# Optimization experiments

Hardware: AMD Instinct MI355X
Metric: run time of the kernel (lower is better)

The kernel has to match this reference:

```python
import jax, jax.numpy as jnp
import numpy as np

D_MODEL = 1024
H = 16
D_K = D_MODEL // H
SEQ = 4096
SIM_WEIGHT = 1.0


def setup_inputs() -> dict:
    key = jax.random.key(0)
    ks = jax.random.split(key, 10)
    s = 1.0 / np.sqrt(D_MODEL)
    return {
        "x": jax.random.normal(ks[0], (SEQ, D_MODEL), dtype=jnp.float32),
        "similarity_matrix": jax.random.normal(ks[1], (SEQ, SEQ), dtype=jnp.float32),
        "w_q": jax.random.normal(ks[2], (D_MODEL, D_MODEL), dtype=jnp.float32) * s,
        "b_q": jnp.zeros((D_MODEL,), dtype=jnp.float32),
        "w_k": jax.random.normal(ks[3], (D_MODEL, D_MODEL), dtype=jnp.float32) * s,
        "b_k": jnp.zeros((D_MODEL,), dtype=jnp.float32),
        "w_v": jax.random.normal(ks[4], (D_MODEL, D_MODEL), dtype=jnp.float32) * s,
        "b_v": jnp.zeros((D_MODEL,), dtype=jnp.float32),
        "w_o": jax.random.normal(ks[5], (D_MODEL, D_MODEL), dtype=jnp.float32) * s,
        "b_o": jnp.zeros((D_MODEL,), dtype=jnp.float32),
    }


def reference(x, similarity_matrix, w_q, b_q, w_k, b_k, w_v, b_v, w_o, b_o):
    # x: [S, D]; project and split heads -> [H, S, d_k]
    q = (x @ w_q.T + b_q).reshape(SEQ, H, D_K).transpose(1, 0, 2)
    k = (x @ w_k.T + b_k).reshape(SEQ, H, D_K).transpose(1, 0, 2)
    v = (x @ w_v.T + b_v).reshape(SEQ, H, D_K).transpose(1, 0, 2)
    # scores: [H, S, S]; additive similarity bias broadcast over heads
    scores = jnp.einsum("hsd,htd->hst", q, k) / jnp.sqrt(jnp.float32(D_K))
    scores = scores + similarity_matrix[None, :, :] * SIM_WEIGHT
    attn = jax.nn.softmax(scores, axis=-1)
    out = jnp.einsum("hst,htd->hsd", attn, v)  # [H, S, d_k]
    out = out.transpose(1, 0, 2).reshape(SEQ, D_MODEL)
    return out @ w_o.T + b_o
```

## Files before the change

kernel.cpp:

```cpp
#include <hip/hip_runtime.h>
#include <hip/hip_bf16.h>

typedef __hip_bfloat16 bf16;
typedef __attribute__((ext_vector_type(8))) short short8;
typedef __attribute__((ext_vector_type(4))) float f32x4;

#define SEQ    4096
#define DMODEL 1024
#define NHEAD  16
#define DKH    64

#define LSTRIDE 72
#define PSTRIDE 72

__device__ __forceinline__ float ldf(const float* p, size_t i) { return p[i]; }
__device__ __forceinline__ float ldf(const bf16*  p, size_t i) { return __bfloat162float(p[i]); }
__device__ __forceinline__ void stf(float* p, size_t i, float v) { p[i] = v; }
__device__ __forceinline__ void stf(bf16*  p, size_t i, float v) { p[i] = __float2bfloat16(v); }

__device__ __forceinline__ short f2bs(float v) {
    bf16 b = __float2bfloat16(v);
    return *(short*)&b;
}

__device__ __forceinline__ short8 lda8(const bf16* p, size_t i) {
    return *(const short8*)(p + i);
}
__device__ __forceinline__ short8 lda8(const float* p, size_t i) {
    float4 a = *(const float4*)(p + i);
    float4 b = *(const float4*)(p + i + 4);
    short8 r;
    r[0] = f2bs(a.x); r[1] = f2bs(a.y); r[2] = f2bs(a.z); r[3] = f2bs(a.w);
    r[4] = f2bs(b.x); r[5] = f2bs(b.y); r[6] = f2bs(b.z); r[7] = f2bs(b.w);
    return r;
}

__device__ __forceinline__ void g2l16(const void* g, void* l) {
    __builtin_amdgcn_global_load_lds(
        (const __attribute__((address_space(1))) unsigned int*)g,
        (__attribute__((address_space(3))) unsigned int*)l, 16, 0, 0);
}

__global__ void detect_dtype(const unsigned short* __restrict__ x, int* __restrict__ flag) {
    int lane = threadIdx.x;
    int cnt = 0;
    for (int i = lane; i < 512; i += 64) {
        int e = (x[i] >> 7) & 0xFF;
        cnt += (e >= 100 && e <= 140) ? 1 : 0;
    }
    #pragma unroll
    for (int off = 32; off; off >>= 1) cnt += __shfl_xor(cnt, off, 64);
    if (lane == 0) *flag = (cnt >= 400) ? 1 : 0;
}

template <bool TRANSC, typename TC>
__device__ void gemm_dma_body(const bf16* __restrict__ A, const bf16* __restrict__ B,
                              const bf16* __restrict__ bias, TC* __restrict__ C,
                              int M, int N, int K, short* As, short* Bs) {
    const int tid = threadIdx.x;
    const int w = tid >> 6, lane = tid & 63, q = lane >> 4, c = lane & 15;
    const int m0 = blockIdx.x * 128, n0 = blockIdx.y * 128;
    const int mb = 64 * (w & 1), nb = 64 * (w >> 1);

    f32x4 acc[4][4] = {};

    for (int k0 = 0; k0 < K; k0 += 64) {
        __syncthreads();
        #pragma unroll
        for (int i = 0; i < 4; ++i) {
            int p = i * 256 + tid;
            int row = p >> 3, pc = p & 7, gc = pc ^ (row & 7);
            g2l16(A + (size_t)(m0 + row) * K + k0 + gc * 8, As + (size_t)p * 8);
            g2l16(B + (size_t)(n0 + row) * K + k0 + gc * 8, Bs + (size_t)p * 8);
        }
        __syncthreads();
        #pragma unroll
        for (int kh = 0; kh < 2; ++kh) {
            short8 af[4], bfr[4];
            #pragma unroll
            for (int i = 0; i < 4; ++i) {
                int row = mb + i * 16 + c;
                af[i] = *(const short8*)&As[row * 64 + (((kh * 4 + q) ^ (row & 7)) << 3)];
            }
            #pragma unroll
            for (int j = 0; j < 4; ++j) {
                int row = nb + j * 16 + c;
                bfr[j] = *(const short8*)&Bs[row * 64 + (((kh * 4 + q) ^ (row & 7)) << 3)];
            }
            #pragma unroll
            for (int i = 0; i < 4; ++i)
                #pragma unroll
                for (int j = 0; j < 4; ++j)
                    acc[i][j] = __builtin_amdgcn_mfma_f32_16x16x32_bf16(af[i], bfr[j], acc[i][j], 0, 0, 0);
        }
    }

    #pragma unroll
    for (int j = 0; j < 4; ++j) {
        int n = n0 + nb + j * 16 + c;
        float bj = __bfloat162float(bias[n]);
        #pragma unroll
        for (int i = 0; i < 4; ++i) {
            if (TRANSC) {
                short4 pk;
                pk.x = f2bs(acc[i][j][0] + bj);
                pk.y = f2bs(acc[i][j][1] + bj);
                pk.z = f2bs(acc[i][j][2] + bj);
                pk.w = f2bs(acc[i][j][3] + bj);
                int m = m0 + mb + i * 16 + q * 4;
                *(short4*)&((bf16*)C)[(size_t)n * M + m] = pk;
            } else {
                #pragma unroll
                for (int t = 0; t < 4; ++t) {
                    int m = m0 + mb + i * 16 + q * 4 + t;
                    stf(C, (size_t)m * N + n, acc[i][j][t] + bj);
                }
            }
        }
    }
}

template <typename TA, typename TB, typename TC, bool TRANSC>
__device__ void gemm_legacy_body(const TA* __restrict__ A, const TB* __restrict__ B,
                                 const TB* __restrict__ bias, TC* __restrict__ C,
                                 int M, int N, int K, short* As, short* Bs) {
    const int tid = threadIdx.x;
    const int w = tid >> 6, lane = tid & 63, q = lane >> 4, c = lane & 15;
    const int m0 = blockIdx.x * 128, n0 = blockIdx.y * 128;
    const int mb = 64 * (w & 1), nb = 64 * (w >> 1);

    f32x4 acc[4][4] = {};

    for (int k0 = 0; k0 < K; k0 += 64) {
        __syncthreads();
        #pragma unroll
        for (int i = 0; i < 4; ++i) {
            int ch = tid + 256 * i;
            int r = ch >> 3, c8 = (ch & 7) * 8;
            *(short8*)&As[r * LSTRIDE + c8] = lda8(A, (size_t)(m0 + r) * K + k0 + c8);
            *(short8*)&Bs[r * LSTRIDE + c8] = lda8(B, (size_t)(n0 + r) * K + k0 + c8);
        }
        __syncthreads();
        #pragma unroll
        for (int kh = 0; kh < 2; ++kh) {
            const int kk = kh * 32 + q * 8;
            short8 af[4], bfr[4];
            #pragma unroll
            for (int i = 0; i < 4; ++i)
                af[i] = *(const short8*)&As[(mb + i * 16 + c) * LSTRIDE + kk];
            #pragma unroll
            for (int j = 0; j < 4; ++j)
                bfr[j] = *(const short8*)&Bs[(nb + j * 16 + c) * LSTRIDE + kk];
            #pragma unroll
            for (int i = 0; i < 4; ++i)
                #pragma unroll
                for (int j = 0; j < 4; ++j)
                    acc[i][j] = __builtin_amdgcn_mfma_f32_16x16x32_bf16(af[i], bfr[j], acc[i][j], 0, 0, 0);
        }
    }

    #pragma unroll
    for (int j = 0; j < 4; ++j) {
        int n = n0 + nb + j * 16 + c;
        float bj = ldf(bias, (size_t)n);
        #pragma unroll
        for (int i = 0; i < 4; ++i) {
            if (TRANSC) {
                short4 pk;
                pk.x = f2bs(acc[i][j][0] + bj);
                pk.y = f2bs(acc[i][j][1] + bj);
                pk.z = f2bs(acc[i][j][2] + bj);
                pk.w = f2bs(acc[i][j][3] + bj);
                int m = m0 + mb + i * 16 + q * 4;
                *(short4*)&((bf16*)C)[(size_t)n * M + m] = pk;
            } else {
                #pragma unroll
                for (int t = 0; t < 4; ++t) {
                    int m = m0 + mb + i * 16 + q * 4 + t;
                    stf(C, (size_t)m * N + n, acc[i][j][t] + bj);
                }
            }
        }
    }
}

__global__ __launch_bounds__(256)
void gemm_proj(const void* __restrict__ A, const void* __restrict__ B,
               const void* __restrict__ bias, bf16* __restrict__ C,
               const int* __restrict__ flag, int M, int N, int K) {
    __shared__ __align__(16) short As[128 * LSTRIDE];
    __shared__ __align__(16) short Bs[128 * LSTRIDE];
    if (*flag)
        gemm_dma_body<false, bf16>((const bf16*)A, (const bf16*)B, (const bf16*)bias, C, M, N, K, As, Bs);
    else
        gemm_legacy_body<float, float, bf16, false>((const float*)A, (const float*)B, (const float*)bias, C, M, N, K, As, Bs);
}

__global__ __launch_bounds__(256)
void gemm_projT(const void* __restrict__ A, const void* __restrict__ B,
                const void* __restrict__ bias, bf16* __restrict__ C,
                const int* __restrict__ flag, int M, int N, int K) {
    __shared__ __align__(16) short As[128 * LSTRIDE];
    __shared__ __align__(16) short Bs[128 * LSTRIDE];
    if (*flag)
        gemm_dma_body<true, bf16>((const bf16*)A, (const bf16*)B, (const bf16*)bias, C, M, N, K, As, Bs);
    else
        gemm_legacy_body<float, float, bf16, true>((const float*)A, (const float*)B, (const float*)bias, C, M, N, K, As, Bs);
}

__global__ __launch_bounds__(256)
void gemm_out(const bf16* __restrict__ A, const void* __restrict__ B,
              const void* __restrict__ bias, void* __restrict__ C,
              const int* __restrict__ flag, int M, int N, int K) {
    __shared__ __align__(16) short As[128 * LSTRIDE];
    __shared__ __align__(16) short Bs[128 * LSTRIDE];
    if (*flag)
        gemm_dma_body<false, bf16>(A, (const bf16*)B, (const bf16*)bias, (bf16*)C, M, N, K, As, Bs);
    else
        gemm_legacy_body<bf16, float, float, false>(A, (const float*)B, (const float*)bias, (float*)C, M, N, K, As, Bs);
}

template <typename TS>
__device__ void flash_body(const bf16* __restrict__ Q, const bf16* __restrict__ Kg,
                           const bf16* __restrict__ VtG, const TS* __restrict__ sim,
                           bf16* __restrict__ O, short* Ps) {
    const int tid = threadIdx.x;
    const int w = tid >> 6, lane = tid & 63, q = lane >> 4, c = lane & 15;
    const int q0 = blockIdx.x * 128, hd = blockIdx.y * DKH;
    const int r0 = q0 + w * 32;

    short8 aq[2][2];
    #pragma unroll
    for (int m = 0; m < 2; ++m)
        #pragma unroll
        for (int kc = 0; kc < 2; ++kc)
            aq[m][kc] = *(const short8*)&Q[(size_t)(r0 + m * 16 + c) * DMODEL + hd + kc * 32 + q * 8];

    const TS* simp[2][4];
    #pragma unroll
    for (int m = 0; m < 2; ++m)
        #pragma unroll
        for (int i = 0; i < 4; ++i)
            simp[m][i] = sim + (size_t)(r0 + m * 16 + q * 4 + i) * SEQ + c;

    f32x4 accO[2][4] = {};
    float Lp[2][4] = {};

    for (int t = 0; t < SEQ / 64; ++t) {
        const int k0 = t * 64;

        short8 bk[4][2];
        #pragma unroll
        for (int f = 0; f < 4; ++f)
            #pragma unroll
            for (int kc = 0; kc < 2; ++kc)
                bk[f][kc] = *(const short8*)&Kg[(size_t)(k0 + f * 16 + c) * DMODEL + hd + kc * 32 + q * 8];

        f32x4 sfr[2][4];
        #pragma unroll
        for (int m = 0; m < 2; ++m)
            #pragma unroll
            for (int f = 0; f < 4; ++f) {
                f32x4 a = {};
                a = __builtin_amdgcn_mfma_f32_16x16x32_bf16(aq[m][0], bk[f][0], a, 0, 0, 0);
                a = __builtin_amdgcn_mfma_f32_16x16x32_bf16(aq[m][1], bk[f][1], a, 0, 0, 0);
                sfr[m][f] = a;
            }

        #pragma unroll
        for (int m = 0; m < 2; ++m)
            #pragma unroll
            for (int f = 0; f < 4; ++f)
                #pragma unroll
                for (int i = 0; i < 4; ++i) {
                    float s = sfr[m][f][i] * 0.125f + ldf(simp[m][i], (size_t)k0 + f * 16);
                    float p = __expf(s);
                    Lp[m][i] += p;
                    Ps[(w * 32 + m * 16 + q * 4 + i) * PSTRIDE + f * 16 + c] = f2bs(p);
                }

        short8 bv[4][2];
        #pragma unroll
        for (int f = 0; f < 4; ++f)
            #pragma unroll
            for (int kc = 0; kc < 2; ++kc)
                bv[f][kc] = *(const short8*)&VtG[(size_t)(hd + f * 16 + c) * SEQ + k0 + kc * 32 + q * 8];

        short8 ap[2][2];
        #pragma unroll
        for (int m = 0; m < 2; ++m)
            #pragma unroll
            for (int kc = 0; kc < 2; ++kc)
                ap[m][kc] = *(const short8*)&Ps[(w * 32 + m * 16 + c) * PSTRIDE + kc * 32 + q * 8];

        #pragma unroll
        for (int m = 0; m < 2; ++m)
            #pragma unroll
            for (int f = 0; f < 4; ++f) {
                accO[m][f] = __builtin_amdgcn_mfma_f32_16x16x32_bf16(ap[m][0], bv[f][0], accO[m][f], 0, 0, 0);
                accO[m][f] = __builtin_amdgcn_mfma_f32_16x16x32_bf16(ap[m][1], bv[f][1], accO[m][f], 0, 0, 0);
            }
    }

    #pragma unroll
    for (int off = 1; off < 16; off <<= 1)
        #pragma unroll
        for (int m = 0; m < 2; ++m)
            #pragma unroll
            for (int i = 0; i < 4; ++i)
                Lp[m][i] += __shfl_xor(Lp[m][i], off, 64);

    #pragma unroll
    for (int m = 0; m < 2; ++m)
        #pragma unroll
        for (int i = 0; i < 4; ++i) {
            float inv = 1.f / Lp[m][i];
            int gr = r0 + m * 16 + q * 4 + i;
            #pragma unroll
            for (int f = 0; f < 4; ++f)
                O[(size_t)gr * DMODEL + hd + f * 16 + c] = __float2bfloat16(accO[m][f][i] * inv);
        }
}

__global__ __launch_bounds__(256)
void flash_mfma(const bf16* __restrict__ Q, const bf16* __restrict__ K,
                const bf16* __restrict__ Vt, const void* __restrict__ sim,
                bf16* __restrict__ O, const int* __restrict__ flag) {
    __shared__ __align__(16) short Ps[128 * PSTRIDE];
    if (*flag)
        flash_body<bf16>(Q, K, Vt, (const bf16*)sim, O, Ps);
    else
        flash_body<float>(Q, K, Vt, (const float*)sim, O, Ps);
}

extern "C" void kernel_launch(void* const* d_in, const int* in_sizes, int n_in,
                              void* d_out, int out_size, void* d_ws, size_t ws_size,
                              hipStream_t stream) {
    int* flagw = (int*)d_ws;
    const int* flag = (const int*)d_ws;
    bf16* Q  = (bf16*)((char*)d_ws + 256);
    bf16* K  = Q + (size_t)SEQ * DMODEL;
    bf16* Vt = K + (size_t)SEQ * DMODEL;
    bf16* O  = Vt + (size_t)SEQ * DMODEL;

    detect_dtype<<<1, 64, 0, stream>>>((const unsigned short*)d_in[0], flagw);

    dim3 gg(SEQ / 128, DMODEL / 128);
    dim3 blk(256);
    gemm_proj <<<gg, blk, 0, stream>>>(d_in[0], d_in[2], d_in[3], Q,  flag, SEQ, DMODEL, DMODEL);
    gemm_proj <<<gg, blk, 0, stream>>>(d_in[0], d_in[4], d_in[5], K,  flag, SEQ, DMODEL, DMODEL);
    gemm_projT<<<gg, blk, 0, stream>>>(d_in[0], d_in[6], d_in[7], Vt, flag, SEQ, DMODEL, DMODEL);

    flash_mfma<<<dim3(SEQ / 128, NHEAD), blk, 0, stream>>>(Q, K, Vt, d_in[1], O, flag);

    gemm_out<<<gg, blk, 0, stream>>>(O, d_in[8], d_in[9], d_out, flag, SEQ, DMODEL, DMODEL);
}
```

Measured before the change: 568.9 us.

## Fuse QKV projections, split flash attention over keys, and shrink output GEMM tiles

The three Q/K/V projection GEMMs become one launch with a 24-column grid, where each block picks its weight, bias and output. Flash attention can now split the key range in two along blockIdx.z. Each half writes unnormalized fp32 partial outputs and row sums, and a separate combine kernel adds them and normalizes. The bf16 output GEMM switches to 64-row tiles so it launches twice as many blocks. The goal is more blocks in flight on the GPU's many compute units. The cost is an extra fp32 partial buffer round-trip and one more kernel launch, and the split path runs only when the workspace is large enough.

```diff
diff --git a/kernel.cpp b/kernel.cpp
--- a/kernel.cpp
+++ b/kernel.cpp
@@ -53,13 +53,13 @@
     if (lane == 0) *flag = (cnt >= 400) ? 1 : 0;
 }
 
-template <bool TRANSC, typename TC>
+template <typename TC>
 __device__ void gemm_dma_body(const bf16* __restrict__ A, const bf16* __restrict__ B,
                               const bf16* __restrict__ bias, TC* __restrict__ C,
-                              int M, int N, int K, short* As, short* Bs) {
+                              int m0, int n0, int M, int N, int K, bool transc,
+                              short* As, short* Bs) {
     const int tid = threadIdx.x;
     const int w = tid >> 6, lane = tid & 63, q = lane >> 4, c = lane & 15;
-    const int m0 = blockIdx.x * 128, n0 = blockIdx.y * 128;
     const int mb = 64 * (w & 1), nb = 64 * (w >> 1);
 
     f32x4 acc[4][4] = {};
@@ -101,7 +101,7 @@
         float bj = __bfloat162float(bias[n]);
         #pragma unroll
         for (int i = 0; i < 4; ++i) {
-            if (TRANSC) {
+            if (transc) {
                 short4 pk;
                 pk.x = f2bs(acc[i][j][0] + bj);
                 pk.y = f2bs(acc[i][j][1] + bj);
@@ -120,13 +120,74 @@
     }
 }
 
-template <typename TA, typename TB, typename TC, bool TRANSC>
+template <typename TC>
+__device__ void gemm_dma64_body(const bf16* __restrict__ A, const bf16* __restrict__ B,
+                                const bf16* __restrict__ bias, TC* __restrict__ C,
+                                int m0, int n0, int M, int N, int K,
+                                short* As, short* Bs) {
+    const int tid = threadIdx.x;
+    const int w = tid >> 6, lane = tid & 63, q = lane >> 4, c = lane & 15;
+    const int nb = 32 * w;
+
+    f32x4 acc[4][2] = {};
+
+    for (int k0 = 0; k0 < K; k0 += 64) {
+        __syncthreads();
+        #pragma unroll
+        for (int i = 0; i < 2; ++i) {
+            int p = i * 256 + tid;
+            int row = p >> 3, pc = p & 7, gc = pc ^ (row & 7);
+            g2l16(A + (size_t)(m0 + row) * K + k0 + gc * 8, As + (size_t)p * 8);
+        }
+        #pragma unroll
+        for (int i = 0; i < 4; ++i) {
+            int p = i * 256 + tid;
+            int row = p >> 3, pc = p & 7, gc = pc ^ (row & 7);
+            g2l16(B + (size_t)(n0 + row) * K + k0 + gc * 8, Bs + (size_t)p * 8);
+        }
+        __syncthreads();
+        #pragma unroll
+        for (int kh = 0; kh < 2; ++kh) {
+            short8 af[4], bfr[2];
+            #pragma unroll
+            for (int i = 0; i < 4; ++i) {
+                int row = i * 16 + c;
+                af[i] = *(const short8*)&As[row * 64 + (((kh * 4 + q) ^ (row & 7)) << 3)];
+            }
+            #pragma unroll
+            for (int j = 0; j < 2; ++j) {
+                int row = nb + j * 16 + c;
+                bfr[j] = *(const short8*)&Bs[row * 64 + (((kh * 4 + q) ^ (row & 7)) << 3)];
+            }
+            #pragma unroll
+            for (int i = 0; i < 4; ++i)
+                #pragma unroll
+                for (int j = 0; j < 2; ++j)
+                    acc[i][j] = __builtin_amdgcn_mfma_f32_16x16x32_bf16(af[i], bfr[j], acc[i][j], 0, 0, 0);
+        }
+    }
+
+    #pragma unroll
+    for (int j = 0; j < 2; ++j) {
+        int n = n0 + nb + j * 16 + c;
+        float bj = __bfloat162float(bias[n]);
+        #pragma unroll
+        for (int i = 0; i < 4; ++i)
+            #pragma unroll
+            for (int t = 0; t < 4; ++t) {
+                int m = m0 + i * 16 + q * 4 + t;
+                stf(C, (size_t)m * N + n, acc[i][j][t] + bj);
+            }
+    }
+}
+
+template <typename TA, typename TB, typename TC>
 __device__ void gemm_legacy_body(const TA* __restrict__ A, const TB* __restrict__ B,
                                  const TB* __restrict__ bias, TC* __restrict__ C,
-                                 int M, int N, int K, short* As, short* Bs) {
+                                 int m0, int n0, int M, int N, int K, bool transc,
+                                 short* As, short* Bs) {
     const int tid = threadIdx.x;
     const int w = tid >> 6, lane = tid & 63, q = lane >> 4, c = lane & 15;
-    const int m0 = blockIdx.x * 128, n0 = blockIdx.y * 128;
     const int mb = 64 * (w & 1), nb = 64 * (w >> 1);
 
     f32x4 acc[4][4] = {};
@@ -165,7 +226,7 @@
         float bj = ldf(bias, (size_t)n);
         #pragma unroll
         for (int i = 0; i < 4; ++i) {
-            if (TRANSC) {
+            if (transc) {
                 short4 pk;
                 pk.x = f2bs(acc[i][j][0] + bj);
                 pk.y = f2bs(acc[i][j][1] + bj);
@@ -185,48 +246,53 @@
 }
 
 __global__ __launch_bounds__(256)
-void gemm_proj(const void* __restrict__ A, const void* __restrict__ B,
-               const void* __restrict__ bias, bf16* __restrict__ C,
-               const int* __restrict__ flag, int M, int N, int K) {
+void gemm_qkv(const void* __restrict__ x,
+              const void* __restrict__ wq, const void* __restrict__ bq,
+              const void* __restrict__ wk, const void* __restrict__ bk,
+              const void* __restrict__ wv, const void* __restrict__ bv,
+              bf16* __restrict__ Q, bf16* __restrict__ K, bf16* __restrict__ Vt,
+              const int* __restrict__ flag) {
     __shared__ __align__(16) short As[128 * LSTRIDE];
     __shared__ __align__(16) short Bs[128 * LSTRIDE];
+    const int sel = blockIdx.y >> 3;
+    const int m0 = blockIdx.x * 128, n0 = (blockIdx.y & 7) * 128;
+    const void* B  = (sel == 0) ? wq : (sel == 1) ? wk : wv;
+    const void* bi = (sel == 0) ? bq : (sel == 1) ? bk : bv;
+    bf16* C        = (sel == 0) ? Q  : (sel == 1) ? K  : Vt;
+    const bool tr = (sel == 2);
     if (*flag)
-        gemm_dma_body<false, bf16>((const bf16*)A, (const bf16*)B, (const bf16*)bias, C, M, N, K, As, Bs);
+        gemm_dma_body<bf16>((const bf16*)x, (const bf16*)B, (const bf16*)bi, C,
+                            m0, n0, SEQ, DMODEL, DMODEL, tr, As, Bs);
     else
-        gemm_legacy_body<float, float, bf16, false>((const float*)A, (const float*)B, (const float*)bias, C, M, N, K, As, Bs);
+        gemm_legacy_body<float, float, bf16>((const float*)x, (const float*)B, (const float*)bi, C,
+                                             m0, n0, SEQ, DMODEL, DMODEL, tr, As, Bs);
 }
 
 __global__ __launch_bounds__(256)
-void gemm_projT(const void* __restrict__ A, const void* __restrict__ B,
-                const void* __restrict__ bias, bf16* __restrict__ C,
+void gemm_out_k(const bf16* __restrict__ A, const void* __restrict__ B,
+                const void* __restrict__ bias, void* __restrict__ C,
                 const int* __restrict__ flag, int M, int N, int K) {
     __shared__ __align__(16) short As[128 * LSTRIDE];
     __shared__ __align__(16) short Bs[128 * LSTRIDE];
-    if (*flag)
-        gemm_dma_body<true, bf16>((const bf16*)A, (const bf16*)B, (const bf16*)bias, C, M, N, K, As, Bs);
-    else
-        gemm_legacy_body<float, float, bf16, true>((const float*)A, (const float*)B, (const float*)bias, C, M, N, K, As, Bs);
-}
-
-__global__ __launch_bounds__(256)
-void gemm_out(const bf16* __restrict__ A, const void* __restrict__ B,
-              const void* __restrict__ bias, void* __restrict__ C,
-              const int* __restrict__ flag, int M, int N, int K) {
-    __shared__ __align__(16) short As[128 * LSTRIDE];
-    __shared__ __align__(16) short Bs[128 * LSTRIDE];
-    if (*flag)
-        gemm_dma_body<false, bf16>(A, (const bf16*)B, (const bf16*)bias, (bf16*)C, M, N, K, As, Bs);
-    else
-        gemm_legacy_body<bf16, float, float, false>(A, (const float*)B, (const float*)bias, (float*)C, M, N, K, As, Bs);
-}
-
-template <typename TS>
+    if (*flag) {
+        gemm_dma64_body<bf16>(A, (const bf16*)B, (const bf16*)bias, (bf16*)C,
+                              blockIdx.x * 64, blockIdx.y * 128, M, N, K, As, Bs);
+    } else {
+        if (blockIdx.x >= (unsigned)(M / 128)) return;
+        gemm_legacy_body<bf16, float, float>(A, (const float*)B, (const float*)bias, (float*)C,
+                                             blockIdx.x * 128, blockIdx.y * 128, M, N, K, false, As, Bs);
+    }
+}
+
+template <typename TS, bool SPLIT>
 __device__ void flash_body(const bf16* __restrict__ Q, const bf16* __restrict__ Kg,
                            const bf16* __restrict__ VtG, const TS* __restrict__ sim,
-                           bf16* __restrict__ O, short* Ps) {
+                           bf16* __restrict__ O, float* __restrict__ Opart,
+                           float* __restrict__ Lpart, short* Ps, int t0, int nt) {
     const int tid = threadIdx.x;
     const int w = tid >> 6, lane = tid & 63, q = lane >> 4, c = lane & 15;
     const int q0 = blockIdx.x * 128, hd = blockIdx.y * DKH;
+    const int kz = blockIdx.z;
     const int r0 = q0 + w * 32;
 
     short8 aq[2][2];
@@ -246,7 +312,7 @@
     f32x4 accO[2][4] = {};
     float Lp[2][4] = {};
 
-    for (int t = 0; t < SEQ / 64; ++t) {
+    for (int t = t0; t < t0 + nt; ++t) {
         const int k0 = t * 64;
 
         short8 bk[4][2];
@@ -310,27 +376,74 @@
             for (int i = 0; i < 4; ++i)
                 Lp[m][i] += __shfl_xor(Lp[m][i], off, 64);
 
-    #pragma unroll
-    for (int m = 0; m < 2; ++m)
-        #pragma unroll
-        for (int i = 0; i < 4; ++i) {
-            float inv = 1.f / Lp[m][i];
-            int gr = r0 + m * 16 + q * 4 + i;
-            #pragma unroll
-            for (int f = 0; f < 4; ++f)
-                O[(size_t)gr * DMODEL + hd + f * 16 + c] = __float2bfloat16(accO[m][f][i] * inv);
-        }
+    if (SPLIT) {
+        #pragma unroll
+        for (int m = 0; m < 2; ++m)
+            #pragma unroll
+            for (int i = 0; i < 4; ++i) {
+                int gr = r0 + m * 16 + q * 4 + i;
+                if (c == 0)
+                    Lpart[((size_t)kz * NHEAD + blockIdx.y) * SEQ + gr] = Lp[m][i];
+                #pragma unroll
+                for (int f = 0; f < 4; ++f)
+                    Opart[((size_t)kz * SEQ + gr) * DMODEL + hd + f * 16 + c] = accO[m][f][i];
+            }
+    } else {
+        #pragma unroll
+        for (int m = 0; m < 2; ++m)
+            #pragma unroll
+            for (int i = 0; i < 4; ++i) {
+                float inv = 1.f / Lp[m][i];
+                int gr = r0 + m * 16 + q * 4 + i;
+                #pragma unroll
+                for (int f = 0; f < 4; ++f)
+                    O[(size_t)gr * DMODEL + hd + f * 16 + c] = __float2bfloat16(accO[m][f][i] * inv);
+            }
+    }
 }
 
 __global__ __launch_bounds__(256)
-void flash_mfma(const bf16* __restrict__ Q, const bf16* __restrict__ K,
-                const bf16* __restrict__ Vt, const void* __restrict__ sim,
-                bf16* __restrict__ O, const int* __restrict__ flag) {
+void flash_split(const bf16* __restrict__ Q, const bf16* __restrict__ K,
+                 const bf16* __restrict__ Vt, const void* __restrict__ sim,
+                 float* __restrict__ Opart, float* __restrict__ Lpart,
+                 const int* __restrict__ flag, int t0mul, int nt) {
+    __shared__ __align__(16) short Ps[128 * PSTRIDE];
+    const int t0 = blockIdx.z * t0mul;
+    if (*flag)
+        flash_body<bf16, true>(Q, K, Vt, (const bf16*)sim, nullptr, Opart, Lpart, Ps, t0, nt);
+    else
+        flash_body<float, true>(Q, K, Vt, (const float*)sim, nullptr, Opart, Lpart, Ps, t0, nt);
+}
+
+__global__ __launch_bounds__(256)
+void flash_ns(const bf16* __restrict__ Q, const bf16* __restrict__ K,
+              const bf16* __restrict__ Vt, const void* __restrict__ sim,
+              bf16* __restrict__ O, const int* __restrict__ flag) {
     __shared__ __align__(16) short Ps[128 * PSTRIDE];
     if (*flag)
-        flash_body<bf16>(Q, K, Vt, (const bf16*)sim, O, Ps);
+        flash_body<bf16, false>(Q, K, Vt, (const bf16*)sim, O, nullptr, nullptr, Ps, 0, SEQ / 64);
     else
-        flash_body<float>(Q, K, Vt, (const float*)sim, O, Ps);
+        flash_body<float, false>(Q, K, Vt, (const float*)sim, O, nullptr, nullptr, Ps, 0, SEQ / 64);
+}
+
+__global__ __launch_bounds__(256)
+void combine_k(const float* __restrict__ Opart, const float* __restrict__ Lpart,
+               bf16* __restrict__ O) {
+    size_t idx = (size_t)blockIdx.x * 256 + threadIdx.x;
+    size_t base = idx * 4;
+    int row = (int)(base >> 10);
+    int d = (int)(base & 1023);
+    int h = d >> 6;
+    const float4 a = *(const float4*)&Opart[base];
+    const float4 b = *(const float4*)&Opart[(size_t)SEQ * DMODEL + base];
+    float L = Lpart[(size_t)h * SEQ + row] + Lpart[(size_t)(NHEAD + h) * SEQ + row];
+    float inv = 1.f / L;
+    short4 pk;
+    pk.x = f2bs((a.x + b.x) * inv);
+    pk.y = f2bs((a.y + b.y) * inv);
+    pk.z = f2bs((a.z + b.z) * inv);
+    pk.w = f2bs((a.w + b.w) * inv);
+    *(short4*)&O[base] = pk;
 }
 
 extern "C" void kernel_launch(void* const* d_in, const int* in_sizes, int n_in,
@@ -342,16 +455,28 @@
     bf16* K  = Q + (size_t)SEQ * DMODEL;
     bf16* Vt = K + (size_t)SEQ * DMODEL;
     bf16* O  = Vt + (size_t)SEQ * DMODEL;
+    float* Lpart = (float*)(O + (size_t)SEQ * DMODEL);
+    float* Opart = Lpart + 2 * (size_t)NHEAD * SEQ;
+
+    const size_t need = 256 + 4 * (size_t)SEQ * DMODEL * sizeof(bf16)
+                      + 2 * (size_t)NHEAD * SEQ * sizeof(float)
+                      + 2 * (size_t)SEQ * DMODEL * sizeof(float);
+    const bool split = (ws_size >= need);
 
     detect_dtype<<<1, 64, 0, stream>>>((const unsigned short*)d_in[0], flagw);
 
-    dim3 gg(SEQ / 128, DMODEL / 128);
     dim3 blk(256);
-    gemm_proj <<<gg, blk, 0, stream>>>(d_in[0], d_in[2], d_in[3], Q,  flag, SEQ, DMODEL, DMODEL);
-    gemm_proj <<<gg, blk, 0, stream>>>(d_in[0], d_in[4], d_in[5], K,  flag, SEQ, DMODEL, DMODEL);
-    gemm_projT<<<gg, blk, 0, stream>>>(d_in[0], d_in[6], d_in[7], Vt, flag, SEQ, DMODEL, DMODEL);
-
-    flash_mfma<<<dim3(SEQ / 128, NHEAD), blk, 0, stream>>>(Q, K, Vt, d_in[1], O, flag);
-
-    gemm_out<<<gg, blk, 0, stream>>>(O, d_in[8], d_in[9], d_out, flag, SEQ, DMODEL, DMODEL);
-}
+    gemm_qkv<<<dim3(SEQ / 128, 24), blk, 0, stream>>>(
+        d_in[0], d_in[2], d_in[3], d_in[4], d_in[5], d_in[6], d_in[7], Q, K, Vt, flag);
+
+    if (split) {
+        flash_split<<<dim3(SEQ / 128, NHEAD, 2), blk, 0, stream>>>(
+            Q, K, Vt, d_in[1], Opart, Lpart, flag, SEQ / 128, SEQ / 128);
+        combine_k<<<dim3(SEQ * DMODEL / 1024), blk, 0, stream>>>(Opart, Lpart, O);
+    } else {
+        flash_ns<<<dim3(SEQ / 128, NHEAD), blk, 0, stream>>>(Q, K, Vt, d_in[1], O, flag);
+    }
+
+    gemm_out_k<<<dim3(SEQ / 64, DMODEL / 128), blk, 0, stream>>>(
+        O, d_in[8], d_in[9], d_out, flag, SEQ, DMODEL, DMODEL);
+}
```

Result: faster. 504.6 us (-11.3%).
